# Performance work log

Hardware: AMD Instinct MI355X
Metric: run time of the kernel (lower is better)

Reference implementation:

```python
import jax, jax.numpy as jnp
import numpy as np

B, D, H, T = 4096, 1024, 1024, 50
FREE_RATIO = 0.0  # default free_running_ratio


def setup_inputs() -> dict:
    key = jax.random.key(0)
    ks = jax.random.split(key, 10)
    s_init = 1.0 / np.sqrt(D)
    s_gru = 1.0 / np.sqrt(H)
    return {
        "ev_context": jax.random.normal(ks[0], (B, D), dtype=jnp.float32),
        "teacher_deltas": jax.random.normal(ks[1], (B, T, 2), dtype=jnp.float32),
        "w_init": jax.random.uniform(ks[2], (H, D), jnp.float32, -s_init, s_init),
        "b_init": jax.random.uniform(ks[3], (H,), jnp.float32, -s_init, s_init),
        "w_ih": jax.random.uniform(ks[4], (3 * H, 2), jnp.float32, -s_gru, s_gru),
        "w_hh": jax.random.uniform(ks[5], (3 * H, H), jnp.float32, -s_gru, s_gru),
        "b_ih": jax.random.uniform(ks[6], (3 * H,), jnp.float32, -s_gru, s_gru),
        "b_hh": jax.random.uniform(ks[7], (3 * H,), jnp.float32, -s_gru, s_gru),
        "w_out": jax.random.uniform(ks[8], (2, H), jnp.float32, -s_gru, s_gru),
        "b_out": jax.random.uniform(ks[9], (2,), jnp.float32, -s_gru, s_gru),
    }


def reference(ev_context, teacher_deltas, w_init, b_init, w_ih, w_hh, b_ih, b_hh, w_out, b_out):
    # h0 = tanh(Linear(ev_context))  -> (B, H)
    h0 = jnp.tanh(ev_context @ w_init.T + b_init)
    prev0 = jnp.zeros((B, 2), dtype=ev_context.dtype)
    # teacher forcing mask: rand(B) < free_running_ratio, drawn per step
    free_mask = jax.random.uniform(jax.random.key(1), (T, B)) < FREE_RATIO
    teach_seq = jnp.swapaxes(teacher_deltas, 0, 1)  # (T, B, 2)

    def step(carry, xs):
        h, prev = carry
        teach_t, free_t = xs
        # PyTorch GRU cell, gate order (r, z, n)
        gx = prev @ w_ih.T + b_ih            # (B, 3H)
        gh = h @ w_hh.T + b_hh               # (B, 3H)
        xr, xz, xn = jnp.split(gx, 3, axis=-1)
        hr, hz, hn = jnp.split(gh, 3, axis=-1)
        r = jax.nn.sigmoid(xr + hr)
        z = jax.nn.sigmoid(xz + hz)
        n = jnp.tanh(xn + r * hn)
        h_new = (1.0 - z) * n + z * h
        delta = h_new @ w_out.T + b_out      # (B, 2)
        prev_next = jnp.where(free_t[:, None], delta, teach_t)
        return (h_new, prev_next), delta

    _, deltas = jax.lax.scan(step, (h0, prev0), (teach_seq, free_mask))
    pred_deltas = jnp.swapaxes(deltas, 0, 1)          # (B, T, 2)
    pred_pos = jnp.cumsum(pred_deltas, axis=1)        # (B, T, 2)
    return pred_deltas, pred_pos
```

## Files before the change

### kernel.cpp

```cpp
#include <hip/hip_runtime.h>
#include <math.h>

#define B_SZ 4096
#define D_SZ 1024
#define H_SZ 1024
#define T_SZ 50

typedef _Float16 f16;
typedef __attribute__((ext_vector_type(8))) _Float16 f16x8;
typedef __attribute__((ext_vector_type(4))) _Float16 f16x4;
typedef __attribute__((ext_vector_type(2))) _Float16 f16x2;
typedef __attribute__((ext_vector_type(4))) float f32x4;
typedef __attribute__((ext_vector_type(4))) float f4;

__device__ __forceinline__ float fast_sigmoid(float x) {
    return 1.0f / (1.0f + __expf(-x));
}
__device__ __forceinline__ float fast_tanh(float x) {
    return 1.0f - 2.0f / (__expf(2.0f * x) + 1.0f);
}

__device__ __forceinline__ void gl_lds16(const void* g, void* l) {
    __builtin_amdgcn_global_load_lds(
        (const __attribute__((address_space(1))) unsigned int*)g,
        (__attribute__((address_space(3))) unsigned int*)l, 16, 0, 0);
}

#define LGKM0() do { asm volatile("s_waitcnt lgkmcnt(0)" ::: "memory"); __builtin_amdgcn_sched_barrier(0); } while (0)

__global__ __launch_bounds__(256) void conv_kernel(
        const float* __restrict__ s, f16* __restrict__ d, int n) {
    int i = (blockIdx.x * 256 + threadIdx.x) * 4;
    if (i < n) {
        f4 v = *(const f4*)&s[i];
        f16x4 o = {(f16)v[0], (f16)v[1], (f16)v[2], (f16)v[3]};
        *(f16x4*)&d[i] = o;
    }
}

__global__ __launch_bounds__(256) void ttrans_kernel(
        const float* __restrict__ teach, f16* __restrict__ tT) {
    int idx = blockIdx.x * 256 + threadIdx.x;
    if (idx >= T_SZ * B_SZ) return;
    int t = idx >> 12, b = idx & 4095;
    float v0 = teach[b * (T_SZ * 2) + t * 2 + 0];
    float v1 = teach[b * (T_SZ * 2) + t * 2 + 1];
    f16x2 o = {(f16)v0, (f16)v1};
    *(f16x2*)&tT[(size_t)idx * 2] = o;
}

__global__ __launch_bounds__(256) void prepack_kernel(
        const float* __restrict__ w, f16* __restrict__ wpk) {
    const int idx = blockIdx.x * 256 + threadIdx.x;
    const int kt = blockIdx.y, jb = blockIdx.z;
    const int row = idx >> 2, s = idx & 3;
    const int g = row >> 6, jj = row & 63;
    const int col = (kt << 5) + ((s ^ ((row >> 1) & 3)) << 3);
    const float* src =
        w + ((size_t)(g << 10) + (jb << 6) + jj) * H_SZ + col;
    f4 v0 = *(const f4*)src;
    f4 v1 = *(const f4*)(src + 4);
    f16x8 o = {(f16)v0[0], (f16)v0[1], (f16)v0[2], (f16)v0[3],
               (f16)v1[0], (f16)v1[1], (f16)v1[2], (f16)v1[3]};
    *(f16x8*)&wpk[((size_t)jb * 32 + kt) * 6144 + idx * 8] = o;
}

__global__ __launch_bounds__(256, 2) void h0_kernel(
        const f16* __restrict__ ev, const f16* __restrict__ wi,
        const float* __restrict__ b_init, f16* __restrict__ hh) {
    __shared__ __align__(16) f16 lds[6144];
    const int tid = threadIdx.x;
    const int lane = tid & 63, wave = tid >> 6;
    const int b0 = blockIdx.y * 128, j0 = blockIdx.x * 64;
    const int wm = wave >> 1, wn = wave & 1;
    const int lrow = lane & 15, quad = lane >> 4;

    const f16* gsrc[3];
    int lbase[3];
    {
        const int row16 = lane >> 2, part = lane & 3;
#pragma unroll
        for (int i = 0; i < 3; ++i) {
            int c = wave + 4 * i;
            if (c < 8) {
                gsrc[i] = ev + (size_t)(b0 + c * 16 + row16) * D_SZ + part * 8;
                lbase[i] = c * 512;
            } else {
                int cc = c - 8;
                gsrc[i] = wi + (size_t)(j0 + cc * 16 + row16) * D_SZ + part * 8;
                lbase[i] = 4096 + cc * 512;
            }
        }
    }

    int offA[4], offB[2];
#pragma unroll
    for (int mi = 0; mi < 4; ++mi)
        offA[mi] = (wm * 64 + mi * 16 + lrow) * 32 + quad * 8;
#pragma unroll
    for (int ni = 0; ni < 2; ++ni)
        offB[ni] = 4096 + (wn * 32 + ni * 16 + lrow) * 32 + quad * 8;

    f32x4 acc[4][2] = {};

    for (int k0 = 0; k0 < D_SZ; k0 += 32) {
        __syncthreads();
#pragma unroll
        for (int i = 0; i < 3; ++i)
            gl_lds16(gsrc[i] + k0, &lds[lbase[i]] + lane * 8);
        __syncthreads();
        f16x8 aa[4], bb[2];
#pragma unroll
        for (int mi = 0; mi < 4; ++mi) aa[mi] = *(const f16x8*)&lds[offA[mi]];
#pragma unroll
        for (int ni = 0; ni < 2; ++ni) bb[ni] = *(const f16x8*)&lds[offB[ni]];
#pragma unroll
        for (int mi = 0; mi < 4; ++mi)
#pragma unroll
            for (int ni = 0; ni < 2; ++ni)
                acc[mi][ni] = __builtin_amdgcn_mfma_f32_16x16x32_f16(
                    aa[mi], bb[ni], acc[mi][ni], 0, 0, 0);
    }

#pragma unroll
    for (int ni = 0; ni < 2; ++ni) {
        const int j = j0 + wn * 32 + ni * 16 + lrow;
        const float bj = b_init[j];
#pragma unroll
        for (int mi = 0; mi < 4; ++mi)
#pragma unroll
            for (int reg = 0; reg < 4; ++reg) {
                const int b = b0 + wm * 64 + mi * 16 + quad * 4 + reg;
                hh[(size_t)b * H_SZ + j] = (f16)tanhf(acc[mi][ni][reg] + bj);
            }
    }
}

__global__ __launch_bounds__(512, 1) void step_kernel(
        const f16* __restrict__ hh, const f16* __restrict__ wpk,
        const float* __restrict__ b_hh, const float* __restrict__ w_ih,
        const float* __restrict__ b_ih, const float* __restrict__ w_out,
        const f16* __restrict__ tT, f16* __restrict__ nhh,
        float* __restrict__ out, const float* __restrict__ partP,
        float* __restrict__ partC, int step_t) {
    constexpr int TILE_E = 14336;
    __shared__ __align__(16) f16 lds[5 * TILE_E];
    const int tid = threadIdx.x;
    const int lane = tid & 63, wave = tid >> 6;
    const int wm = wave >> 1, wn = wave & 1;
    const int id = blockIdx.x;
    const int xcd = id & 7, slot = id >> 3;
    const int bx = (xcd & 1) * 8 + (slot & 7);
    const int by = (xcd >> 1) * 4 + (slot >> 3);
    const int b0 = by * 256, j0 = bx * 64;
    const int lrow = lane & 15, quad = lane >> 4;

    if (step_t > 0 && bx == 0) {
        const int rr = tid >> 1, cc = tid & 1;
        const int b = b0 + rr;
        float s = 0.f;
#pragma unroll
        for (int x = 0; x < 16; ++x) s += partP[x * 8192 + b * 2 + cc];
        out[b * (T_SZ * 2) + (step_t - 1) * 2 + cc] = s;
    }

    const f16* ga[4];
    const f16* gb;
    {
        const int r = tid >> 2;
        const int cs = ((tid & 3) ^ ((tid >> 3) & 3)) * 8;
#pragma unroll
        for (int i = 0; i < 4; ++i)
            ga[i] = hh + (size_t)(b0 + i * 64 + r) * H_SZ + cs;
        gb = wpk + (size_t)bx * (32 * 6144);
    }
    auto issueT = [&](int kt, int sb) {
        if (tid < 256) {
#pragma unroll
            for (int i = 0; i < 4; ++i)
                gl_lds16(ga[i] + kt * 32, &lds[sb + i * 2048 + tid * 8]);
#pragma unroll
            for (int i = 0; i < 3; ++i)
                gl_lds16(gb + kt * 6144 + i * 2048 + tid * 8,
                         &lds[sb + 8192 + i * 2048 + tid * 8]);
        }
    };

    const int swz = (quad ^ ((lrow >> 1) & 3)) * 8;
    int offA[4], offB[6];
#pragma unroll
    for (int mi = 0; mi < 4; ++mi)
        offA[mi] = (wm * 64 + mi * 16 + lrow) * 32 + swz;
#pragma unroll
    for (int f = 0; f < 6; ++f)
        offB[f] = 8192 + ((f >> 1) * 64 + wn * 32 + (f & 1) * 16 + lrow) * 32 + swz;

    f32x4 acc[3][4][2] = {};

    issueT(0, 0);
    issueT(1, TILE_E);
    issueT(2, 2 * TILE_E);
    issueT(3, 3 * TILE_E);

    int rb = 0, sb = 4 * TILE_E;
    for (int tt = 0; tt < 32; ++tt) {
        if (tt < 29)       asm volatile("s_waitcnt vmcnt(21)" ::: "memory");
        else if (tt == 29) asm volatile("s_waitcnt vmcnt(14)" ::: "memory");
        else if (tt == 30) asm volatile("s_waitcnt vmcnt(7)" ::: "memory");
        else               asm volatile("s_waitcnt vmcnt(0)" ::: "memory");
        __builtin_amdgcn_s_barrier();
        asm volatile("" ::: "memory");
        f16x8 aa[4], bv[6];
#pragma unroll
        for (int mi = 0; mi < 4; ++mi)
            aa[mi] = *(const f16x8*)&lds[rb + offA[mi]];
#pragma unroll
        for (int f = 0; f < 6; ++f)
            bv[f] = *(const f16x8*)&lds[rb + offB[f]];
        if (tt < 28) issueT(tt + 4, sb);
        LGKM0();
        __builtin_amdgcn_s_setprio(1);
#pragma unroll
        for (int f = 0; f < 6; ++f) {
            const int g = f >> 1, ni = f & 1;
#pragma unroll
            for (int mi = 0; mi < 4; ++mi)
                acc[g][mi][ni] = __builtin_amdgcn_mfma_f32_16x16x32_f16(
                    aa[mi], bv[f], acc[g][mi][ni], 0, 0, 0);
        }
        __builtin_amdgcn_s_setprio(0);
        rb += TILE_E; if (rb == 5 * TILE_E) rb = 0;
        sb += TILE_E; if (sb == 5 * TILE_E) sb = 0;
    }

    float p0[4][4], p1[4][4];
#pragma unroll
    for (int mi = 0; mi < 4; ++mi)
#pragma unroll
        for (int reg = 0; reg < 4; ++reg) {
            const int b = b0 + wm * 64 + mi * 16 + quad * 4 + reg;
            if (step_t > 0) {
                f16x2 tv = *(const f16x2*)&tT[((size_t)(step_t - 1) * B_SZ + b) * 2];
                p0[mi][reg] = (float)tv[0];
                p1[mi][reg] = (float)tv[1];
            } else {
                p0[mi][reg] = 0.f;
                p1[mi][reg] = 0.f;
            }
        }

    float s0[4][4] = {}, s1[4][4] = {};
#pragma unroll
    for (int ni = 0; ni < 2; ++ni) {
        const int j = j0 + wn * 32 + ni * 16 + lrow;
        const float wr0 = w_ih[(0 * H_SZ + j) * 2 + 0];
        const float wr1 = w_ih[(0 * H_SZ + j) * 2 + 1];
        const float wz0 = w_ih[(1 * H_SZ + j) * 2 + 0];
        const float wz1 = w_ih[(1 * H_SZ + j) * 2 + 1];
        const float wn0 = w_ih[(2 * H_SZ + j) * 2 + 0];
        const float wn1 = w_ih[(2 * H_SZ + j) * 2 + 1];
        const float br = b_ih[0 * H_SZ + j] + b_hh[0 * H_SZ + j];
        const float bz = b_ih[1 * H_SZ + j] + b_hh[1 * H_SZ + j];
        const float bn = b_ih[2 * H_SZ + j];
        const float hbn = b_hh[2 * H_SZ + j];
        const float wo0 = w_out[j], wo1 = w_out[H_SZ + j];
#pragma unroll
        for (int mi = 0; mi < 4; ++mi) {
#pragma unroll
            for (int reg = 0; reg < 4; ++reg) {
                const int b = b0 + wm * 64 + mi * 16 + quad * 4 + reg;
                const float hr = acc[0][mi][ni][reg];
                const float hz = acc[1][mi][ni][reg];
                const float hn_ = acc[2][mi][ni][reg] + hbn;
                const float xr = wr0 * p0[mi][reg] + wr1 * p1[mi][reg] + br;
                const float xz = wz0 * p0[mi][reg] + wz1 * p1[mi][reg] + bz;
                const float xn = wn0 * p0[mi][reg] + wn1 * p1[mi][reg] + bn;
                const float r = fast_sigmoid(xr + hr);
                const float z = fast_sigmoid(xz + hz);
                const float n = fast_tanh(xn + r * hn_);
                const size_t idx = (size_t)b * H_SZ + j;
                const float hold = (float)hh[idx];
                const float hnew = (1.0f - z) * n + z * hold;
                nhh[idx] = (f16)hnew;
                s0[mi][reg] += hnew * wo0;
                s1[mi][reg] += hnew * wo1;
            }
        }
    }

    float ra[4][4], rc[4][4];
#pragma unroll
    for (int mi = 0; mi < 4; ++mi)
#pragma unroll
        for (int reg = 0; reg < 4; ++reg) {
            float a = s0[mi][reg], c = s1[mi][reg];
#pragma unroll
            for (int m = 1; m < 16; m <<= 1) {
                a += __shfl_xor(a, m);
                c += __shfl_xor(c, m);
            }
            ra[mi][reg] = a;
            rc[mi][reg] = c;
        }
    float* red = (float*)lds;
    if (wn == 1 && lrow == 0) {
#pragma unroll
        for (int mi = 0; mi < 4; ++mi)
#pragma unroll
            for (int reg = 0; reg < 4; ++reg) {
                const int key = wm * 64 + mi * 16 + quad * 4 + reg;
                red[key * 2 + 0] = ra[mi][reg];
                red[key * 2 + 1] = rc[mi][reg];
            }
    }
    __syncthreads();
    if (wn == 0 && lrow == 0) {
#pragma unroll
        for (int mi = 0; mi < 4; ++mi)
#pragma unroll
            for (int reg = 0; reg < 4; ++reg) {
                const int key = wm * 64 + mi * 16 + quad * 4 + reg;
                const int b = b0 + key;
                partC[bx * 8192 + b * 2 + 0] = ra[mi][reg] + red[key * 2 + 0];
                partC[bx * 8192 + b * 2 + 1] = rc[mi][reg] + red[key * 2 + 1];
            }
    }
}

__global__ __launch_bounds__(256) void final_kernel(
        float* __restrict__ out, float* __restrict__ pos,
        const float* __restrict__ b_out, const float* __restrict__ partLast) {
    int idx = blockIdx.x * 256 + threadIdx.x;
    if (idx >= B_SZ * 2) return;
    int b = idx >> 1, c = idx & 1;
    float bc = b_out[c];
    float acc = 0.0f;
    for (int t = 0; t < T_SZ - 1; ++t) {
        float d = out[b * (T_SZ * 2) + t * 2 + c] + bc;
        out[b * (T_SZ * 2) + t * 2 + c] = d;
        acc += d;
        pos[b * (T_SZ * 2) + t * 2 + c] = acc;
    }
    float s = 0.f;
#pragma unroll
    for (int x = 0; x < 16; ++x) s += partLast[x * 8192 + b * 2 + c];
    float d = s + bc;
    out[b * (T_SZ * 2) + (T_SZ - 1) * 2 + c] = d;
    acc += d;
    pos[b * (T_SZ * 2) + (T_SZ - 1) * 2 + c] = acc;
}

extern "C" void kernel_launch(void* const* d_in, const int* in_sizes, int n_in,
                              void* d_out, int out_size, void* d_ws, size_t ws_size,
                              hipStream_t stream) {
    const float* ev     = (const float*)d_in[0];
    const float* teach  = (const float*)d_in[1];
    const float* w_init = (const float*)d_in[2];
    const float* b_init = (const float*)d_in[3];
    const float* w_ih   = (const float*)d_in[4];
    const float* w_hh   = (const float*)d_in[5];
    const float* b_ih   = (const float*)d_in[6];
    const float* b_hh   = (const float*)d_in[7];
    const float* w_out  = (const float*)d_in[8];
    const float* b_out  = (const float*)d_in[9];

    float* out = (float*)d_out;
    float* pos = out + (size_t)B_SZ * T_SZ * 2;

    f16* ws = (f16*)d_ws;
    f16* hA    = ws;
    f16* hB    = hA + (size_t)B_SZ * H_SZ;
    f16* wpk   = hB + (size_t)B_SZ * H_SZ;
    f16* winit = wpk + (size_t)3 * H_SZ * H_SZ;
    f16* evf   = hB;
    f16* tT    = winit;
    float* pA  = (float*)(winit + 417792);
    float* pB  = pA + 131072;

    conv_kernel<<<(H_SZ * D_SZ) / 1024, 256, 0, stream>>>(w_init, winit, H_SZ * D_SZ);
    conv_kernel<<<(B_SZ * D_SZ) / 1024, 256, 0, stream>>>(ev, evf, B_SZ * D_SZ);
    prepack_kernel<<<dim3(3, 32, 16), 256, 0, stream>>>(w_hh, wpk);

    dim3 g0(H_SZ / 64, B_SZ / 128);
    h0_kernel<<<g0, 256, 0, stream>>>(evf, winit, b_init, hA);

    ttrans_kernel<<<(T_SZ * B_SZ + 255) / 256, 256, 0, stream>>>(teach, tT);

    f16 *hc = hA, *hn = hB;
    for (int t = 0; t < T_SZ; ++t) {
        float* partC = (t & 1) ? pB : pA;
        float* partP = (t & 1) ? pA : pB;
        step_kernel<<<256, 512, 0, stream>>>(hc, wpk, b_hh, w_ih, b_ih, w_out,
                                             tT, hn, out, partP, partC, t);
        f16* tmp = hc; hc = hn; hn = tmp;
    }
    final_kernel<<<(B_SZ * 2 + 255) / 256, 256, 0, stream>>>(out, pos, b_out, pB);
}
```

Measured before the change: 1.988 ms.

## Fuse all GRU time steps into one persistent cooperative kernel with row-group barriers

Replaces the 50 separate step_kernel launches with a single cooperative persistent kernel that loops over time steps. Between steps, blocks synchronize through per-batch-row-group atomic counters, waiting only on the 16 blocks that share the same hidden-state rows, not on a full grid barrier. This removes per-launch overhead and the drain/fill gaps between launches, and lets independent row groups advance at different rates. In exchange it adds spin-wait barrier costs and fences, requires all 256 blocks to be co-resident, and distributes the output reduction across blocks. The per-gate weights and biases are hoisted into registers once, which raises register pressure.

```diff
diff --git a/kernel.cpp b/kernel.cpp
--- a/kernel.cpp
+++ b/kernel.cpp
@@ -136,13 +136,12 @@
     }
 }
 
-__global__ __launch_bounds__(512, 1) void step_kernel(
-        const f16* __restrict__ hh, const f16* __restrict__ wpk,
+__global__ __launch_bounds__(512, 1) void steps_kernel(
+        f16* hA, f16* hB, const f16* __restrict__ wpk,
         const float* __restrict__ b_hh, const float* __restrict__ w_ih,
         const float* __restrict__ b_ih, const float* __restrict__ w_out,
-        const f16* __restrict__ tT, f16* __restrict__ nhh,
-        float* __restrict__ out, const float* __restrict__ partP,
-        float* __restrict__ partC, int step_t) {
+        const f16* __restrict__ tT, float* out, float* pA, float* pB,
+        int* barc) {
     constexpr int TILE_E = 14336;
     __shared__ __align__(16) f16 lds[5 * TILE_E];
     const int tid = threadIdx.x;
@@ -155,36 +154,10 @@
     const int b0 = by * 256, j0 = bx * 64;
     const int lrow = lane & 15, quad = lane >> 4;
 
-    if (step_t > 0 && bx == 0) {
-        const int rr = tid >> 1, cc = tid & 1;
-        const int b = b0 + rr;
-        float s = 0.f;
-#pragma unroll
-        for (int x = 0; x < 16; ++x) s += partP[x * 8192 + b * 2 + cc];
-        out[b * (T_SZ * 2) + (step_t - 1) * 2 + cc] = s;
-    }
-
-    const f16* ga[4];
-    const f16* gb;
-    {
-        const int r = tid >> 2;
-        const int cs = ((tid & 3) ^ ((tid >> 3) & 3)) * 8;
-#pragma unroll
-        for (int i = 0; i < 4; ++i)
-            ga[i] = hh + (size_t)(b0 + i * 64 + r) * H_SZ + cs;
-        gb = wpk + (size_t)bx * (32 * 6144);
-    }
-    auto issueT = [&](int kt, int sb) {
-        if (tid < 256) {
-#pragma unroll
-            for (int i = 0; i < 4; ++i)
-                gl_lds16(ga[i] + kt * 32, &lds[sb + i * 2048 + tid * 8]);
-#pragma unroll
-            for (int i = 0; i < 3; ++i)
-                gl_lds16(gb + kt * 6144 + i * 2048 + tid * 8,
-                         &lds[sb + 8192 + i * 2048 + tid * 8]);
-        }
-    };
+    const f16* gb = wpk + (size_t)bx * (32 * 6144);
+    const int srow = tid >> 2;
+    const int scol = ((tid & 3) ^ ((tid >> 3) & 3)) * 8;
+    const size_t aoff = (size_t)(b0 + srow) * H_SZ + scol;
 
     const int swz = (quad ^ ((lrow >> 1) & 3)) * 8;
     int offA[4], offB[6];
@@ -195,135 +168,190 @@
     for (int f = 0; f < 6; ++f)
         offB[f] = 8192 + ((f >> 1) * 64 + wn * 32 + (f & 1) * 16 + lrow) * 32 + swz;
 
-    f32x4 acc[3][4][2] = {};
-
-    issueT(0, 0);
-    issueT(1, TILE_E);
-    issueT(2, 2 * TILE_E);
-    issueT(3, 3 * TILE_E);
-
-    int rb = 0, sb = 4 * TILE_E;
-    for (int tt = 0; tt < 32; ++tt) {
-        if (tt < 29)       asm volatile("s_waitcnt vmcnt(21)" ::: "memory");
-        else if (tt == 29) asm volatile("s_waitcnt vmcnt(14)" ::: "memory");
-        else if (tt == 30) asm volatile("s_waitcnt vmcnt(7)" ::: "memory");
-        else               asm volatile("s_waitcnt vmcnt(0)" ::: "memory");
-        __builtin_amdgcn_s_barrier();
-        asm volatile("" ::: "memory");
-        f16x8 aa[4], bv[6];
-#pragma unroll
-        for (int mi = 0; mi < 4; ++mi)
-            aa[mi] = *(const f16x8*)&lds[rb + offA[mi]];
-#pragma unroll
-        for (int f = 0; f < 6; ++f)
-            bv[f] = *(const f16x8*)&lds[rb + offB[f]];
-        if (tt < 28) issueT(tt + 4, sb);
-        LGKM0();
-        __builtin_amdgcn_s_setprio(1);
-#pragma unroll
-        for (int f = 0; f < 6; ++f) {
-            const int g = f >> 1, ni = f & 1;
-#pragma unroll
-            for (int mi = 0; mi < 4; ++mi)
-                acc[g][mi][ni] = __builtin_amdgcn_mfma_f32_16x16x32_f16(
-                    aa[mi], bv[f], acc[g][mi][ni], 0, 0, 0);
-        }
-        __builtin_amdgcn_s_setprio(0);
-        rb += TILE_E; if (rb == 5 * TILE_E) rb = 0;
-        sb += TILE_E; if (sb == 5 * TILE_E) sb = 0;
-    }
-
-    float p0[4][4], p1[4][4];
-#pragma unroll
-    for (int mi = 0; mi < 4; ++mi)
-#pragma unroll
-        for (int reg = 0; reg < 4; ++reg) {
-            const int b = b0 + wm * 64 + mi * 16 + quad * 4 + reg;
-            if (step_t > 0) {
-                f16x2 tv = *(const f16x2*)&tT[((size_t)(step_t - 1) * B_SZ + b) * 2];
-                p0[mi][reg] = (float)tv[0];
-                p1[mi][reg] = (float)tv[1];
-            } else {
-                p0[mi][reg] = 0.f;
-                p1[mi][reg] = 0.f;
-            }
-        }
-
-    float s0[4][4] = {}, s1[4][4] = {};
+    float ewr0[2], ewr1[2], ewz0[2], ewz1[2], ewn0[2], ewn1[2];
+    float ebr[2], ebz[2], ebn[2], ehbn[2], ewo0[2], ewo1[2];
 #pragma unroll
     for (int ni = 0; ni < 2; ++ni) {
         const int j = j0 + wn * 32 + ni * 16 + lrow;
-        const float wr0 = w_ih[(0 * H_SZ + j) * 2 + 0];
-        const float wr1 = w_ih[(0 * H_SZ + j) * 2 + 1];
-        const float wz0 = w_ih[(1 * H_SZ + j) * 2 + 0];
-        const float wz1 = w_ih[(1 * H_SZ + j) * 2 + 1];
-        const float wn0 = w_ih[(2 * H_SZ + j) * 2 + 0];
-        const float wn1 = w_ih[(2 * H_SZ + j) * 2 + 1];
-        const float br = b_ih[0 * H_SZ + j] + b_hh[0 * H_SZ + j];
-        const float bz = b_ih[1 * H_SZ + j] + b_hh[1 * H_SZ + j];
-        const float bn = b_ih[2 * H_SZ + j];
-        const float hbn = b_hh[2 * H_SZ + j];
-        const float wo0 = w_out[j], wo1 = w_out[H_SZ + j];
-#pragma unroll
-        for (int mi = 0; mi < 4; ++mi) {
+        ewr0[ni] = w_ih[(0 * H_SZ + j) * 2 + 0];
+        ewr1[ni] = w_ih[(0 * H_SZ + j) * 2 + 1];
+        ewz0[ni] = w_ih[(1 * H_SZ + j) * 2 + 0];
+        ewz1[ni] = w_ih[(1 * H_SZ + j) * 2 + 1];
+        ewn0[ni] = w_ih[(2 * H_SZ + j) * 2 + 0];
+        ewn1[ni] = w_ih[(2 * H_SZ + j) * 2 + 1];
+        ebr[ni] = b_ih[0 * H_SZ + j] + b_hh[0 * H_SZ + j];
+        ebz[ni] = b_ih[1 * H_SZ + j] + b_hh[1 * H_SZ + j];
+        ebn[ni] = b_ih[2 * H_SZ + j];
+        ehbn[ni] = b_hh[2 * H_SZ + j];
+        ewo0[ni] = w_out[j];
+        ewo1[ni] = w_out[H_SZ + j];
+    }
+
+    for (int t = 0; t < T_SZ; ++t) {
+        const f16* hc = (t & 1) ? hB : hA;
+        f16* hn = (t & 1) ? hA : hB;
+        const float* partP = (t & 1) ? pA : pB;
+        float* partC = (t & 1) ? pB : pA;
+
+        if (t > 0 && tid < 32) {
+            const int b = b0 + bx * 16 + (tid >> 1), cc = tid & 1;
+            float s = 0.f;
+#pragma unroll
+            for (int x = 0; x < 16; ++x) s += partP[x * 8192 + b * 2 + cc];
+            out[b * (T_SZ * 2) + (t - 1) * 2 + cc] = s;
+        }
+
+        const f16* ga[4];
+#pragma unroll
+        for (int i = 0; i < 4; ++i) ga[i] = hc + aoff + (size_t)i * 64 * H_SZ;
+
+        auto issueT = [&](int kt, int sb) {
+            if (tid < 256) {
+#pragma unroll
+                for (int i = 0; i < 4; ++i)
+                    gl_lds16(ga[i] + kt * 32, &lds[sb + i * 2048 + tid * 8]);
+#pragma unroll
+                for (int i = 0; i < 3; ++i)
+                    gl_lds16(gb + kt * 6144 + i * 2048 + tid * 8,
+                             &lds[sb + 8192 + i * 2048 + tid * 8]);
+            }
+        };
+
+        f32x4 acc[3][4][2] = {};
+
+        issueT(0, 0);
+        issueT(1, TILE_E);
+        issueT(2, 2 * TILE_E);
+        issueT(3, 3 * TILE_E);
+
+        int rb = 0, sb = 4 * TILE_E;
+        for (int tt = 0; tt < 32; ++tt) {
+            if (tt < 29)       asm volatile("s_waitcnt vmcnt(21)" ::: "memory");
+            else if (tt == 29) asm volatile("s_waitcnt vmcnt(14)" ::: "memory");
+            else if (tt == 30) asm volatile("s_waitcnt vmcnt(7)" ::: "memory");
+            else               asm volatile("s_waitcnt vmcnt(0)" ::: "memory");
+            __builtin_amdgcn_s_barrier();
+            asm volatile("" ::: "memory");
+            f16x8 aa[4], bv[6];
+#pragma unroll
+            for (int mi = 0; mi < 4; ++mi)
+                aa[mi] = *(const f16x8*)&lds[rb + offA[mi]];
+#pragma unroll
+            for (int f = 0; f < 6; ++f)
+                bv[f] = *(const f16x8*)&lds[rb + offB[f]];
+            if (tt < 28) issueT(tt + 4, sb);
+            LGKM0();
+            __builtin_amdgcn_s_setprio(1);
+#pragma unroll
+            for (int f = 0; f < 6; ++f) {
+                const int g = f >> 1, ni = f & 1;
+#pragma unroll
+                for (int mi = 0; mi < 4; ++mi)
+                    acc[g][mi][ni] = __builtin_amdgcn_mfma_f32_16x16x32_f16(
+                        aa[mi], bv[f], acc[g][mi][ni], 0, 0, 0);
+            }
+            __builtin_amdgcn_s_setprio(0);
+            rb += TILE_E; if (rb == 5 * TILE_E) rb = 0;
+            sb += TILE_E; if (sb == 5 * TILE_E) sb = 0;
+        }
+
+        float p0[4][4], p1[4][4];
+#pragma unroll
+        for (int mi = 0; mi < 4; ++mi)
 #pragma unroll
             for (int reg = 0; reg < 4; ++reg) {
                 const int b = b0 + wm * 64 + mi * 16 + quad * 4 + reg;
-                const float hr = acc[0][mi][ni][reg];
-                const float hz = acc[1][mi][ni][reg];
-                const float hn_ = acc[2][mi][ni][reg] + hbn;
-                const float xr = wr0 * p0[mi][reg] + wr1 * p1[mi][reg] + br;
-                const float xz = wz0 * p0[mi][reg] + wz1 * p1[mi][reg] + bz;
-                const float xn = wn0 * p0[mi][reg] + wn1 * p1[mi][reg] + bn;
-                const float r = fast_sigmoid(xr + hr);
-                const float z = fast_sigmoid(xz + hz);
-                const float n = fast_tanh(xn + r * hn_);
-                const size_t idx = (size_t)b * H_SZ + j;
-                const float hold = (float)hh[idx];
-                const float hnew = (1.0f - z) * n + z * hold;
-                nhh[idx] = (f16)hnew;
-                s0[mi][reg] += hnew * wo0;
-                s1[mi][reg] += hnew * wo1;
-            }
-        }
-    }
-
-    float ra[4][4], rc[4][4];
-#pragma unroll
-    for (int mi = 0; mi < 4; ++mi)
-#pragma unroll
-        for (int reg = 0; reg < 4; ++reg) {
-            float a = s0[mi][reg], c = s1[mi][reg];
-#pragma unroll
-            for (int m = 1; m < 16; m <<= 1) {
-                a += __shfl_xor(a, m);
-                c += __shfl_xor(c, m);
-            }
-            ra[mi][reg] = a;
-            rc[mi][reg] = c;
-        }
-    float* red = (float*)lds;
-    if (wn == 1 && lrow == 0) {
+                if (t > 0) {
+                    f16x2 tv = *(const f16x2*)&tT[((size_t)(t - 1) * B_SZ + b) * 2];
+                    p0[mi][reg] = (float)tv[0];
+                    p1[mi][reg] = (float)tv[1];
+                } else {
+                    p0[mi][reg] = 0.f;
+                    p1[mi][reg] = 0.f;
+                }
+            }
+
+        float s0[4][4] = {}, s1[4][4] = {};
+#pragma unroll
+        for (int ni = 0; ni < 2; ++ni) {
+            const int j = j0 + wn * 32 + ni * 16 + lrow;
+#pragma unroll
+            for (int mi = 0; mi < 4; ++mi) {
+#pragma unroll
+                for (int reg = 0; reg < 4; ++reg) {
+                    const int b = b0 + wm * 64 + mi * 16 + quad * 4 + reg;
+                    const float hr = acc[0][mi][ni][reg];
+                    const float hz = acc[1][mi][ni][reg];
+                    const float hn_ = acc[2][mi][ni][reg] + ehbn[ni];
+                    const float xr = ewr0[ni] * p0[mi][reg] + ewr1[ni] * p1[mi][reg] + ebr[ni];
+                    const float xz = ewz0[ni] * p0[mi][reg] + ewz1[ni] * p1[mi][reg] + ebz[ni];
+                    const float xn = ewn0[ni] * p0[mi][reg] + ewn1[ni] * p1[mi][reg] + ebn[ni];
+                    const float r = fast_sigmoid(xr + hr);
+                    const float z = fast_sigmoid(xz + hz);
+                    const float n = fast_tanh(xn + r * hn_);
+                    const size_t idx = (size_t)b * H_SZ + j;
+                    const float hold = (float)hc[idx];
+                    const float hnew = (1.0f - z) * n + z * hold;
+                    hn[idx] = (f16)hnew;
+                    s0[mi][reg] += hnew * ewo0[ni];
+                    s1[mi][reg] += hnew * ewo1[ni];
+                }
+            }
+        }
+
+        float ra[4][4], rc[4][4];
 #pragma unroll
         for (int mi = 0; mi < 4; ++mi)
 #pragma unroll
             for (int reg = 0; reg < 4; ++reg) {
-                const int key = wm * 64 + mi * 16 + quad * 4 + reg;
-                red[key * 2 + 0] = ra[mi][reg];
-                red[key * 2 + 1] = rc[mi][reg];
-            }
-    }
-    __syncthreads();
-    if (wn == 0 && lrow == 0) {
-#pragma unroll
-        for (int mi = 0; mi < 4; ++mi)
-#pragma unroll
-            for (int reg = 0; reg < 4; ++reg) {
-                const int key = wm * 64 + mi * 16 + quad * 4 + reg;
-                const int b = b0 + key;
-                partC[bx * 8192 + b * 2 + 0] = ra[mi][reg] + red[key * 2 + 0];
-                partC[bx * 8192 + b * 2 + 1] = rc[mi][reg] + red[key * 2 + 1];
-            }
+                float a = s0[mi][reg], c = s1[mi][reg];
+#pragma unroll
+                for (int m = 1; m < 16; m <<= 1) {
+                    a += __shfl_xor(a, m);
+                    c += __shfl_xor(c, m);
+                }
+                ra[mi][reg] = a;
+                rc[mi][reg] = c;
+            }
+        float* red = (float*)lds;
+        __syncthreads();
+        if (wn == 1 && lrow == 0) {
+#pragma unroll
+            for (int mi = 0; mi < 4; ++mi)
+#pragma unroll
+                for (int reg = 0; reg < 4; ++reg) {
+                    const int key = wm * 64 + mi * 16 + quad * 4 + reg;
+                    red[key * 2 + 0] = ra[mi][reg];
+                    red[key * 2 + 1] = rc[mi][reg];
+                }
+        }
+        __syncthreads();
+        if (wn == 0 && lrow == 0) {
+#pragma unroll
+            for (int mi = 0; mi < 4; ++mi)
+#pragma unroll
+                for (int reg = 0; reg < 4; ++reg) {
+                    const int key = wm * 64 + mi * 16 + quad * 4 + reg;
+                    const int b = b0 + key;
+                    partC[bx * 8192 + b * 2 + 0] = ra[mi][reg] + red[key * 2 + 0];
+                    partC[bx * 8192 + b * 2 + 1] = rc[mi][reg] + red[key * 2 + 1];
+                }
+        }
+
+        if (t < T_SZ - 1) {
+            __syncthreads();
+            if (tid == 0) {
+                __builtin_amdgcn_fence(__ATOMIC_RELEASE, "agent");
+                __hip_atomic_fetch_add(&barc[by], 1, __ATOMIC_RELAXED,
+                                       __HIP_MEMORY_SCOPE_AGENT);
+                const int target = 16 * (t + 1);
+                while (__hip_atomic_load(&barc[by], __ATOMIC_RELAXED,
+                                         __HIP_MEMORY_SCOPE_AGENT) < target)
+                    __builtin_amdgcn_s_sleep(2);
+                __builtin_amdgcn_fence(__ATOMIC_ACQUIRE, "agent");
+            }
+            __syncthreads();
+        }
     }
 }
 
@@ -376,6 +404,7 @@
     f16* tT    = winit;
     float* pA  = (float*)(winit + 417792);
     float* pB  = pA + 131072;
+    int* barc  = (int*)(winit + 942080);
 
     conv_kernel<<<(H_SZ * D_SZ) / 1024, 256, 0, stream>>>(w_init, winit, H_SZ * D_SZ);
     conv_kernel<<<(B_SZ * D_SZ) / 1024, 256, 0, stream>>>(ev, evf, B_SZ * D_SZ);
@@ -385,14 +414,14 @@
     h0_kernel<<<g0, 256, 0, stream>>>(evf, winit, b_init, hA);
 
     ttrans_kernel<<<(T_SZ * B_SZ + 255) / 256, 256, 0, stream>>>(teach, tT);
-
-    f16 *hc = hA, *hn = hB;
-    for (int t = 0; t < T_SZ; ++t) {
-        float* partC = (t & 1) ? pB : pA;
-        float* partP = (t & 1) ? pA : pB;
-        step_kernel<<<256, 512, 0, stream>>>(hc, wpk, b_hh, w_ih, b_ih, w_out,
-                                             tT, hn, out, partP, partC, t);
-        f16* tmp = hc; hc = hn; hn = tmp;
-    }
+    hipMemsetAsync(barc, 0, 16 * sizeof(int), stream);
+
+    const float* bhh_p = b_hh; const float* wih_p = w_ih;
+    const float* bih_p = b_ih; const float* wout_p = w_out;
+    void* args[] = {&hA, &hB, &wpk, &bhh_p, &wih_p, &bih_p, &wout_p,
+                    &tT, &out, &pA, &pB, &barc};
+    hipLaunchCooperativeKernel((const void*)steps_kernel, dim3(256), dim3(512),
+                               args, 0, stream);
+
     final_kernel<<<(B_SZ * 2 + 255) / 256, 256, 0, stream>>>(out, pos, b_out, pB);
 }
```

After: 3.221 ms. 62.1% more time.
